# Optimization experiments

Measured on AMD Instinct MI355X. Metric: run time of the kernel, lower is better.

The kernel has to match this reference:

```python
import jax, jax.numpy as jnp
import numpy as np

AXIS = 0
INPUT_SHAPE = (50000, 1024)
N_IDX = 131072

def setup_inputs() -> dict:
    key = jax.random.key(0)
    k1, k2 = jax.random.split(key)
    grad_last = jax.random.normal(k1, (N_IDX, INPUT_SHAPE[1]), dtype=jnp.float32)
    indices = jax.random.randint(k2, (N_IDX,), 0, INPUT_SHAPE[0], dtype=jnp.int64)
    return {"grad_last": grad_last, "indices": indices}

def reference(grad_last, indices):
    # Gather backward: scatter-add grad_last slices along AXIS into zeros(INPUT_SHAPE).
    # Equivalent to the torch module's per-index loop, done in one fused scatter-add.
    g = jnp.moveaxis(grad_last, AXIS, 0)  # [n_idx, ...rest]
    out_shape = (INPUT_SHAPE[AXIS],) + g.shape[1:]
    out = jnp.zeros(out_shape, dtype=grad_last.dtype).at[indices].add(g)
    return jnp.moveaxis(out, 0, AXIS)
```

## Files before the change

### kernel.cpp

```cpp
#include <hip/hip_runtime.h>
#include <hip/hip_bf16.h>


#define NCOLS 1024
#define C4 (NCOLS / 4)
#define CAP 15

typedef float f4 __attribute__((ext_vector_type(4)));

__global__ void fill_kernel(const int* __restrict__ idx, int* __restrict__ meta,
                            int* __restrict__ ovf_list, int* __restrict__ ovf_cnt,
                            int n) {
    int i = blockIdx.x * blockDim.x + threadIdx.x;
    if (i >= n) return;
    int row = idx[i];
    int local = atomicAdd(&meta[(size_t)row * 16], 1);
    if (local < CAP) {
        meta[(size_t)row * 16 + 1 + local] = i;
    } else {
        int s = atomicAdd(ovf_cnt, 1);
        ovf_list[s] = i;
    }
}

__global__ __launch_bounds__(256) void gather_kernel(
    const f4* __restrict__ grad, const int4* __restrict__ meta4,
    const int* __restrict__ idx, const int* __restrict__ ovf_list,
    const int* __restrict__ ovf_cnt, f4* __restrict__ out) {
    int row = blockIdx.x;
    int tid = threadIdx.x;

    int4 m0 = meta4[(size_t)row * 4 + 0];
    int4 m1 = meta4[(size_t)row * 4 + 1];
    int4 m2 = meta4[(size_t)row * 4 + 2];
    int4 m3 = meta4[(size_t)row * 4 + 3];
    int n_raw = m0.x;
    int n = n_raw > CAP ? CAP : n_raw;
    int g[CAP] = {m0.y, m0.z, m0.w,
                  m1.x, m1.y, m1.z, m1.w,
                  m2.x, m2.y, m2.z, m2.w,
                  m3.x, m3.y, m3.z, m3.w};

    f4 v[CAP];
    #pragma unroll
    for (int k = 0; k < CAP; ++k)
        if (k < n) v[k] = __builtin_nontemporal_load(&grad[(size_t)g[k] * C4 + tid]);

    f4 acc = {0.f, 0.f, 0.f, 0.f};
    #pragma unroll
    for (int k = 0; k < CAP; ++k)
        if (k < n) acc += v[k];

    if (n_raw > CAP) {
        int no = *ovf_cnt;
        for (int e = 0; e < no; ++e) {
            int i = ovf_list[e];
            if (idx[i] == row)
                acc += __builtin_nontemporal_load(&grad[(size_t)i * C4 + tid]);
        }
    }

    __builtin_nontemporal_store(acc, &out[(size_t)row * C4 + tid]);
}

__global__ __launch_bounds__(256) void scatter_atomic_kernel(
    const float4* __restrict__ grad, const int* __restrict__ idx,
    float* __restrict__ out, int n_idx) {
    int row = blockIdx.x;
    if (row >= n_idx) return;
    int c4 = threadIdx.x;
    int target = idx[row];
    float4 v = grad[(size_t)row * C4 + c4];
    float* o = out + (size_t)target * NCOLS + (size_t)c4 * 4;
    atomicAdd(o + 0, v.x);
    atomicAdd(o + 1, v.y);
    atomicAdd(o + 2, v.z);
    atomicAdd(o + 3, v.w);
}

extern "C" void kernel_launch(void* const* d_in, const int* in_sizes, int n_in,
                              void* d_out, int out_size, void* d_ws, size_t ws_size,
                              hipStream_t stream) {
    const float4* grad = (const float4*)d_in[0];
    const int* idx = (const int*)d_in[1];

    int n_idx = in_sizes[1];
    int nrows = out_size / NCOLS;

    size_t need = ((size_t)nrows * 16 + 1 + n_idx) * sizeof(int);
    if (ws_size < need) {
        hipMemsetAsync(d_out, 0, (size_t)out_size * sizeof(float), stream);
        scatter_atomic_kernel<<<n_idx, 256, 0, stream>>>(grad, idx, (float*)d_out, n_idx);
        return;
    }

    int* meta     = (int*)d_ws;
    int* ovf_cnt  = meta + (size_t)nrows * 16;
    int* ovf_list = ovf_cnt + 1;

    hipMemsetAsync(meta, 0, ((size_t)nrows * 16 + 1) * sizeof(int), stream);

    int blk = 256;
    fill_kernel<<<(n_idx + blk - 1) / blk, blk, 0, stream>>>(
        idx, meta, ovf_list, ovf_cnt, n_idx);
    gather_kernel<<<nrows, 256, 0, stream>>>((const f4*)grad, (const int4*)meta,
                                             idx, ovf_list, ovf_cnt,
                                             (f4*)d_out);
}
```

Measured before the change: 145.4 us.

## Fuse memset, bucket fill and gather into one persistent kernel with grid barriers

Replaces the metadata memset plus two separate kernel launches with a single persistent kernel of 1024 blocks. It zeroes metadata in-kernel, fills the buckets, and uses software grid barriers (atomic counter with spin and timeout) between phases. It then grid-strides over output rows, prefetching the next row's metadata while loads are in flight. This removes launch gaps and the larger memset, but depends on all 1024 blocks being co-resident. Correctness relies on a timeout-based barrier that could silently break if blocks are not scheduled together.

```diff
diff --git a/kernel.cpp b/kernel.cpp
--- a/kernel.cpp
+++ b/kernel.cpp
@@ -5,62 +5,97 @@
 #define NCOLS 1024
 #define C4 (NCOLS / 4)
 #define CAP 15
+#define NBLK 1024
+#define NTHR 256
 
 typedef float f4 __attribute__((ext_vector_type(4)));
 
-__global__ void fill_kernel(const int* __restrict__ idx, int* __restrict__ meta,
-                            int* __restrict__ ovf_list, int* __restrict__ ovf_cnt,
-                            int n) {
-    int i = blockIdx.x * blockDim.x + threadIdx.x;
-    if (i >= n) return;
-    int row = idx[i];
-    int local = atomicAdd(&meta[(size_t)row * 16], 1);
-    if (local < CAP) {
-        meta[(size_t)row * 16 + 1 + local] = i;
-    } else {
-        int s = atomicAdd(ovf_cnt, 1);
-        ovf_list[s] = i;
+__device__ __forceinline__ void grid_bar(int* cnt) {
+    __syncthreads();
+    if (threadIdx.x == 0) {
+        __threadfence();
+        atomicAdd(cnt, 1);
+        unsigned long long t0 = __builtin_amdgcn_s_memrealtime();
+        while (__hip_atomic_load(cnt, __ATOMIC_ACQUIRE,
+                                 __HIP_MEMORY_SCOPE_AGENT) < NBLK) {
+            __builtin_amdgcn_s_sleep(2);
+            if (__builtin_amdgcn_s_memrealtime() - t0 > 20000000ull) break;
+        }
     }
+    __syncthreads();
 }
 
-__global__ __launch_bounds__(256) void gather_kernel(
-    const f4* __restrict__ grad, const int4* __restrict__ meta4,
-    const int* __restrict__ idx, const int* __restrict__ ovf_list,
-    const int* __restrict__ ovf_cnt, f4* __restrict__ out) {
+__global__ __launch_bounds__(NTHR, 4) void fused_kernel(
+    const f4* __restrict__ grad, const int* __restrict__ idx,
+    int* __restrict__ meta, int* __restrict__ ovf_list,
+    int* __restrict__ ovf_cnt, int* __restrict__ bar,
+    f4* __restrict__ out, int n_idx, int nrows) {
+    int tid = threadIdx.x;
+    int gtid = blockIdx.x * NTHR + tid;
+    const int gstride = NBLK * NTHR;
+
+    int n_int4 = nrows * 4;
+    int4 z = {0, 0, 0, 0};
+    for (int i = gtid; i < n_int4; i += gstride) ((int4*)meta)[i] = z;
+    if (gtid == 0) *ovf_cnt = 0;
+    grid_bar(bar);
+
+    for (int i = gtid; i < n_idx; i += gstride) {
+        int row = idx[i];
+        int local = atomicAdd(&meta[(size_t)row * 16], 1);
+        if (local < CAP) {
+            meta[(size_t)row * 16 + 1 + local] = i;
+        } else {
+            int s = atomicAdd(ovf_cnt, 1);
+            ovf_list[s] = i;
+        }
+    }
+    grid_bar(bar + 1);
+
+    const int4* meta4 = (const int4*)meta;
     int row = blockIdx.x;
-    int tid = threadIdx.x;
-
     int4 m0 = meta4[(size_t)row * 4 + 0];
     int4 m1 = meta4[(size_t)row * 4 + 1];
     int4 m2 = meta4[(size_t)row * 4 + 2];
     int4 m3 = meta4[(size_t)row * 4 + 3];
-    int n_raw = m0.x;
-    int n = n_raw > CAP ? CAP : n_raw;
-    int g[CAP] = {m0.y, m0.z, m0.w,
-                  m1.x, m1.y, m1.z, m1.w,
-                  m2.x, m2.y, m2.z, m2.w,
-                  m3.x, m3.y, m3.z, m3.w};
+    while (row < nrows) {
+        int nxt = row + NBLK;
+        int n_raw = m0.x;
+        int n = n_raw > CAP ? CAP : n_raw;
+        int g[CAP] = {m0.y, m0.z, m0.w,
+                      m1.x, m1.y, m1.z, m1.w,
+                      m2.x, m2.y, m2.z, m2.w,
+                      m3.x, m3.y, m3.z, m3.w};
 
-    f4 v[CAP];
-    #pragma unroll
-    for (int k = 0; k < CAP; ++k)
-        if (k < n) v[k] = __builtin_nontemporal_load(&grad[(size_t)g[k] * C4 + tid]);
+        f4 v[CAP];
+        #pragma unroll
+        for (int k = 0; k < CAP; ++k)
+            if (k < n) v[k] = __builtin_nontemporal_load(&grad[(size_t)g[k] * C4 + tid]);
 
-    f4 acc = {0.f, 0.f, 0.f, 0.f};
-    #pragma unroll
-    for (int k = 0; k < CAP; ++k)
-        if (k < n) acc += v[k];
+        if (nxt < nrows) {
+            m0 = meta4[(size_t)nxt * 4 + 0];
+            m1 = meta4[(size_t)nxt * 4 + 1];
+            m2 = meta4[(size_t)nxt * 4 + 2];
+            m3 = meta4[(size_t)nxt * 4 + 3];
+        }
 
-    if (n_raw > CAP) {
-        int no = *ovf_cnt;
-        for (int e = 0; e < no; ++e) {
-            int i = ovf_list[e];
-            if (idx[i] == row)
-                acc += __builtin_nontemporal_load(&grad[(size_t)i * C4 + tid]);
+        f4 acc = {0.f, 0.f, 0.f, 0.f};
+        #pragma unroll
+        for (int k = 0; k < CAP; ++k)
+            if (k < n) acc += v[k];
+
+        if (n_raw > CAP) {
+            int no = *ovf_cnt;
+            for (int e = 0; e < no; ++e) {
+                int i = ovf_list[e];
+                if (idx[i] == row)
+                    acc += __builtin_nontemporal_load(&grad[(size_t)i * C4 + tid]);
+            }
         }
+
+        __builtin_nontemporal_store(acc, &out[(size_t)row * C4 + tid]);
+        row = nxt;
     }
-
-    __builtin_nontemporal_store(acc, &out[(size_t)row * C4 + tid]);
 }
 
 __global__ __launch_bounds__(256) void scatter_atomic_kernel(
@@ -81,29 +116,28 @@
 extern "C" void kernel_launch(void* const* d_in, const int* in_sizes, int n_in,
                               void* d_out, int out_size, void* d_ws, size_t ws_size,
                               hipStream_t stream) {
-    const float4* grad = (const float4*)d_in[0];
+    const f4* grad = (const f4*)d_in[0];
     const int* idx = (const int*)d_in[1];
+    f4* out = (f4*)d_out;
 
     int n_idx = in_sizes[1];
     int nrows = out_size / NCOLS;
 
-    size_t need = ((size_t)nrows * 16 + 1 + n_idx) * sizeof(int);
+    size_t need = ((size_t)nrows * 16 + 1 + n_idx + 2) * sizeof(int);
     if (ws_size < need) {
         hipMemsetAsync(d_out, 0, (size_t)out_size * sizeof(float), stream);
-        scatter_atomic_kernel<<<n_idx, 256, 0, stream>>>(grad, idx, (float*)d_out, n_idx);
+        scatter_atomic_kernel<<<n_idx, 256, 0, stream>>>(
+            (const float4*)d_in[0], idx, (float*)d_out, n_idx);
         return;
     }
 
     int* meta     = (int*)d_ws;
     int* ovf_cnt  = meta + (size_t)nrows * 16;
     int* ovf_list = ovf_cnt + 1;
+    int* bar      = ovf_list + n_idx;
 
-    hipMemsetAsync(meta, 0, ((size_t)nrows * 16 + 1) * sizeof(int), stream);
+    hipMemsetAsync(bar, 0, 2 * sizeof(int), stream);
 
-    int blk = 256;
-    fill_kernel<<<(n_idx + blk - 1) / blk, blk, 0, stream>>>(
-        idx, meta, ovf_list, ovf_cnt, n_idx);
-    gather_kernel<<<nrows, 256, 0, stream>>>((const f4*)grad, (const int4*)meta,
-                                             idx, ovf_list, ovf_cnt,
-                                             (f4*)d_out);
+    fused_kernel<<<NBLK, NTHR, 0, stream>>>(grad, idx, meta, ovf_list,
+                                            ovf_cnt, bar, out, n_idx, nrows);
 }
```

After: 347.9 us. +139.3%, slower.
